# Performance work log

Measured on AMD Instinct MI355X. Metric: run time of the kernel, lower is better.

## Reference

```python
import jax, jax.numpy as jnp
import numpy as np
from jax import lax

B, N, FIN, T, K, FC, FT = 8, 2048, 3, 12, 3, 64, 64


def _conv2d(x, w, b, pad):
    # x [B,C,N,T], w [O,I,1,kw], NCHW conv
    y = lax.conv_general_dilated(x, w, (1, 1), pad,
                                 dimension_numbers=('NCHW', 'OIHW', 'NCHW'))
    return y + b[None, :, None, None]


def _spatial_att(h, W, a, alpha, concat):
    # GAT-style dense attention. h [B,N,Fin], W [Fin,D], a [2D,1]
    D = W.shape[1]
    Wh = h @ W                                             # [B,N,D]
    e = jax.nn.leaky_relu(Wh @ a[:D] + jnp.swapaxes(Wh @ a[D:], 1, 2), alpha)  # [B,N,N]
    att = jax.nn.softmax(jax.nn.sigmoid(e), axis=1)        # softmax over dim=1 (as in torch)
    hp = jnp.einsum('bij,bjd->bid', att, Wh)
    return jax.nn.elu(hp) if concat else hp


def setup_inputs() -> dict:
    key = jax.random.key(0)
    ks = jax.random.split(key, 24)
    rnd = lambda i, shape, scale=1.0: (jax.random.normal(ks[i], shape, dtype=jnp.float32) * scale)
    FTm = FC * T  # 768 spatial-attention feature dim
    D = FTm // 2
    return {
        'x': rnd(0, (B, N, FIN, T)),
        'cheb': rnd(1, (K, N, N), 1.0 / np.sqrt(N)),
        'Gamma': rnd(2, (K, FIN, FC), 1.0 / np.sqrt(FIN)),
        'W_heads': rnd(3, (2, FTm, D), 1.0 / np.sqrt(FTm)),
        'a_heads': rnd(4, (2, 2 * D, 1), 1.0 / np.sqrt(2 * D)),
        'W_out': rnd(5, (FTm, FTm), 1.0 / np.sqrt(FTm)),
        'a_out': rnd(6, (2 * FTm, 1), 1.0 / np.sqrt(2 * FTm)),
        'U1': rnd(7, (FT, FT), 1.0 / np.sqrt(FT)),
        'U2': rnd(8, (FT,), 1.0 / np.sqrt(FT)),
        'U3': rnd(9, (FT,), 1.0 / np.sqrt(FT)),
        'be': rnd(10, (1, T, T), 0.1),
        'Ve': rnd(11, (T, T), 1.0 / np.sqrt(T)),
        'time_w': rnd(12, (FT, FC, 1, 3), 1.0 / np.sqrt(3 * FC)),
        'time_b': rnd(13, (FT,), 0.01),
        'res_w': rnd(14, (FT, FIN, 1, 1), 1.0 / np.sqrt(FIN)),
        'res_b': rnd(15, (FT,), 0.01),
        'back_w': rnd(16, (FT, FC, 1, 3), 1.0 / np.sqrt(3 * FC)),
        'back_b': rnd(17, (FT,), 0.01),
        'fore_w': rnd(18, (FT, FC, 1, 3), 1.0 / np.sqrt(3 * FC)),
        'fore_b': rnd(19, (FT,), 0.01),
        'ln_g': jnp.ones((FT,), jnp.float32),
        'ln_b': jnp.zeros((FT,), jnp.float32),
    }


def reference(x, cheb, Gamma, W_heads, a_heads, W_out, a_out, U1, U2, U3, be, Ve,
              time_w, time_b, res_w, res_b, back_w, back_b, fore_w, fore_b, ln_g, ln_b):
    b, n, fin, t = x.shape
    k_ = cheb.shape[0]
    fc = Gamma.shape[2]
    # ChebNetII interpolation coefficients T_k(x_j), x_j = cos((j+0.5)pi/K) -> [j,k]
    jj = np.arange(k_)
    cxj = jnp.asarray(np.cos(np.outer((jj + 0.5) * np.pi / k_, np.arange(k_))), x.dtype)
    lhs = jnp.einsum('jio,jk->kio', Gamma, cxj)                         # [K,Fin,Fc]
    rhs = jnp.einsum('bnit,knm->kbmit', x, cheb)                        # [K,B,N,Fin,T]
    spatial_gcn = jax.nn.relu((2.0 / (k_ + 1)) * jnp.einsum('kbmit,kio->bmot', rhs, lhs))  # [B,N,Fc,T]

    # Spatial transformer: 2 GAT heads + output attention
    h = spatial_gcn.reshape(b, n, fc * t)
    heads = jax.vmap(lambda W, a: _spatial_att(h, W, a, 0.1, True))(W_heads, a_heads)  # [H,B,N,D]
    hcat = jnp.transpose(heads, (1, 2, 0, 3)).reshape(b, n, -1)
    gcn_SAt = jax.nn.relu(_spatial_att(hcat, W_out, a_out, 0.1, False)).reshape(b, n, fc, t)

    # Temporal conv (1x3, pad 1)
    tc = _conv2d(jnp.transpose(gcn_SAt, (0, 2, 1, 3)), time_w, time_b, ((0, 0), (1, 1)))
    tc = jnp.transpose(tc, (0, 2, 1, 3))                                # [B,N,Ft,T]

    # Temporal attention
    lhs_t = jnp.einsum('bnft,fg,g->btn', tc, U1, U2)                    # [B,T,N]
    rhs_t = jnp.einsum('f,bnft->bnt', U3, tc)                           # [B,N,T]
    prod = jnp.einsum('bsn,bnt->bst', lhs_t, rhs_t)                     # [B,T,T]
    E = jnp.einsum('is,bst->bit', Ve, jax.nn.sigmoid(prod + be))
    E = jax.nn.softmax(E, axis=1)
    tcn = jnp.einsum('bnft,bts->bnfs', tc, E)                           # [B,N,Ft,T]

    # Residual (1x1 conv) + LayerNorm over channel dim
    x_res = _conv2d(jnp.transpose(x, (0, 2, 1, 3)), res_w, res_b, ((0, 0), (0, 0)))
    x_res = jnp.transpose(x_res, (0, 2, 1, 3))                          # [B,N,Ft,T]
    z = jnp.transpose(jax.nn.relu(x_res + tcn), (0, 3, 1, 2))           # [B,T,N,Ft]
    mu = z.mean(-1, keepdims=True)
    var = z.var(-1, keepdims=True)
    z = (z - mu) / jnp.sqrt(var + 1e-5) * ln_g + ln_b
    result = jnp.transpose(z, (0, 2, 3, 1))                             # [B,N,Ft,T]

    rp = jnp.transpose(result, (0, 2, 1, 3))
    backcast = jnp.transpose(_conv2d(rp, back_w, back_b, ((0, 0), (1, 1))), (0, 2, 1, 3))
    forecast = jnp.transpose(_conv2d(rp, fore_w, fore_b, ((0, 0), (1, 1))), (0, 2, 1, 3))
    return (backcast, forecast)
```

## Files before the change

### kernel.cpp

```cpp
#include <hip/hip_runtime.h>


typedef unsigned short u16;
typedef __bf16 bf16x8 __attribute__((ext_vector_type(8)));
typedef float f32x4 __attribute__((ext_vector_type(4)));
typedef u16 u16x8 __attribute__((ext_vector_type(8)));

__device__ __forceinline__ u16 f2b(float f) {
  union { float f; unsigned u; } v; v.f = f;
  unsigned u = v.u;
  u = u + 0x7FFFu + ((u >> 16) & 1u);
  return (u16)(u >> 16);
}
__device__ __forceinline__ float b2f(u16 h) {
  union { unsigned u; float f; } v; v.u = ((unsigned)h) << 16; return v.f;
}
__device__ __forceinline__ float qfun(float x) {
  float e = x > 0.f ? x : 0.1f * x;
  float s = 1.f / (1.f + __expf(-e));
  return __expf(s);
}

#define GLOAD16(g, l) __builtin_amdgcn_global_load_lds( \
    (__attribute__((address_space(1))) void*)(g),       \
    (__attribute__((address_space(3))) void*)(l), 16, 0, 0)

constexpr size_t OFF_LHS     = 0x0;
constexpr size_t OFF_U1U2    = 0x1000;
constexpr size_t OFF_BIASBIG = 0x1100;
constexpr size_t OFF_FH      = 0x3000;
constexpr size_t OFF_GH      = 0x23000;
constexpr size_t OFF_RDH     = 0x43000;
constexpr size_t OFF_FO      = 0x63000;
constexpr size_t OFF_GO      = 0x73000;
constexpr size_t OFF_RDO     = 0x83000;
constexpr size_t OFF_LHST    = 0x93000;
constexpr size_t OFF_RHST    = 0x153000;
constexpr size_t OFF_PROD    = 0x213000;
constexpr size_t OFF_E       = 0x215000;
constexpr size_t OFF_WCATT   = 0x220000;
constexpr size_t OFF_WOUTT   = 0x340000;
constexpr size_t OFF_WTBIG   = 0x460000;
constexpr size_t OFF_XCOLT   = 0x580000;
constexpr size_t OFF_CHEBT   = 0x700000;
constexpr size_t OFF_C1      = 0x1F00000;
constexpr size_t OFF_H       = 0x4300000;
constexpr size_t OFF_P       = 0x700000;
constexpr size_t OFF_WHCATT  = 0x5B00000;
constexpr size_t OFF_HCAT    = 0x7300000;
constexpr size_t OFF_WHOUTT  = 0x5B00000;
constexpr size_t OFF_GCNB    = 0x7300000;
constexpr size_t OFF_WBFBIG  = 0x8B00000;
constexpr size_t OFF_TCS     = 0x700000;
constexpr size_t OFF_RESULTB = 0x3700000;
constexpr size_t WS_NEEDED   = 0x8D40000;

struct GemmP {
  const u16* A; const u16* BT;
  long sA, sB;
  int K, lda, ldb;
  int swz, splitK;
  float* Cf; long sCf; int ldcf;
  u16* Cb;  long sCb; int ldcb;
  u16* CbT; int ldcT; long sCbT;
  const float* bias;
  float* outB; float* outF;
};

template <int EPI>
__global__ __launch_bounds__(256, 2) void gemm_bf16(GemmP p) {
  constexpr int SMEM_U16 = (EPI == 1) ? (128 * 136) : 8192;
  __shared__ u16 smem[SMEM_U16];
  u16* As = smem;
  u16* Bs = smem + 4096;
  const int tid  = threadIdx.x;
  const int lane = tid & 63;
  const int wid  = tid >> 6;
  const int wm = wid >> 1, wn = wid & 1;
  const int z = blockIdx.z;

  long m0, n0;
  if (p.swz) {
    int nT = gridDim.x;
    int nwg = nT * gridDim.y;
    int lin = blockIdx.x + nT * blockIdx.y;
    int q = nwg >> 3;
    int swz = (lin & 7) * q + (lin >> 3);
    m0 = (long)(swz / nT) * 128;
    n0 = (long)(swz % nT) * 128;
  } else {
    m0 = (long)blockIdx.x * 128;
    n0 = (long)blockIdx.y * 128;
  }

  const int K = p.K;
  long aBase, bBase;
  if (p.splitK) {
    int kz = z >> 2, ch = z & 3;
    aBase = (long)kz * p.sA + (long)ch * 512;
    bBase = (long)ch * 512;
  } else {
    aBase = (long)z * p.sA;
    bBase = (long)z * p.sB;
  }
  const u16* Ab = p.A + aBase + m0 * p.lda;
  const u16* Bb = p.BT + bBase + n0 * p.ldb;

  const int srow = wid * 32 + (lane >> 2);
  const int skk  = (lane & 3) * 8;
  const u16* aP0 = Ab + (long)srow * p.lda + skk;
  const u16* aP1 = aP0 + (long)16 * p.lda;
  const u16* bP0 = Bb + (long)srow * p.ldb + skk;
  const u16* bP1 = bP0 + (long)16 * p.ldb;
  u16* lA0 = &As[(wid * 2 + 0) * 512];
  u16* lA1 = &As[(wid * 2 + 1) * 512];
  u16* lB0 = &Bs[(wid * 2 + 0) * 512];
  u16* lB1 = &Bs[(wid * 2 + 1) * 512];

  f32x4 acc[4][4];
  f32x4 zero = {0.f, 0.f, 0.f, 0.f};
#pragma unroll
  for (int i = 0; i < 4; ++i)
#pragma unroll
    for (int j = 0; j < 4; ++j) acc[i][j] = zero;

  const int aoff = (wm * 64 + (lane & 15)) * 32 + (lane >> 4) * 8;
  const int boff = (wn * 64 + (lane & 15)) * 32 + (lane >> 4) * 8;

  for (int k0 = 0; k0 < K; k0 += 32) {
    GLOAD16(aP0 + k0, lA0);
    GLOAD16(aP1 + k0, lA1);
    GLOAD16(bP0 + k0, lB0);
    GLOAD16(bP1 + k0, lB1);
    __syncthreads();
    bf16x8 av[4], bv[4];
#pragma unroll
    for (int mi = 0; mi < 4; ++mi) av[mi] = *(const bf16x8*)&As[aoff + mi * 512];
#pragma unroll
    for (int ni = 0; ni < 4; ++ni) bv[ni] = *(const bf16x8*)&Bs[boff + ni * 512];
#pragma unroll
    for (int mi = 0; mi < 4; ++mi)
#pragma unroll
      for (int ni = 0; ni < 4; ++ni)
        acc[mi][ni] = __builtin_amdgcn_mfma_f32_16x16x32_bf16(av[mi], bv[ni], acc[mi][ni], 0, 0, 0);
    __syncthreads();
  }

  if constexpr (EPI == 1) {
#pragma unroll
    for (int mi = 0; mi < 4; ++mi)
#pragma unroll
      for (int ni = 0; ni < 4; ++ni) {
        int cl = wn * 64 + ni * 16 + (lane & 15);
        int mlb = wm * 64 + mi * 16 + ((lane >> 4) << 2);
#pragma unroll
        for (int r = 0; r < 4; ++r)
          smem[cl * 136 + mlb + r] = f2b(acc[mi][ni][r]);
      }
    __syncthreads();
    int c = tid >> 1, half = tid & 1;
    long bat = m0 >> 11;
    u16* dst = p.CbT + bat * p.sCbT + (long)(n0 + c) * p.ldcT + (m0 & 2047) + half * 64;
    const u16* srcp = &smem[c * 136 + half * 64];
#pragma unroll
    for (int j = 0; j < 64; j += 8)
      *(u16x8*)(dst + j) = *(const u16x8*)(srcp + j);
    return;
  }

#pragma unroll
  for (int mi = 0; mi < 4; ++mi) {
    long rb0 = m0 + wm * 64 + mi * 16 + ((lane >> 4) << 2);
#pragma unroll
    for (int ni = 0; ni < 4; ++ni) {
      int col = (int)n0 + wn * 64 + ni * 16 + (lane & 15);
#pragma unroll
      for (int r = 0; r < 4; ++r) {
        float v = acc[mi][ni][r];
        long row = rb0 + r;
        if constexpr (EPI == 0) {
          p.Cf[(long)z * p.sCf + row * p.ldcf + col] = v;
        } else if constexpr (EPI == 2) {
          float e = v > 0.f ? v : expm1f(v);
          p.Cb[(long)z * p.sCb + row * p.ldcb + col] = f2b(e);
        } else if constexpr (EPI == 6) {
          p.Cf[row * 768 + col] = v + p.bias[col & 63];
        } else if constexpr (EPI == 7) {
          float vb = v + p.bias[col];
          if (col < 768) p.outB[row * 768 + col] = vb;
          else           p.outF[row * 768 + (col - 768)] = vb;
        } else {
          p.Cb[(long)z * p.sCb + row * p.ldcb + col] = f2b(fmaxf(v, 0.f));
        }
      }
    }
  }
}

__global__ void k_prep(const float* Gamma, const float* U1, const float* U2,
                       const float* back_b, const float* fore_b,
                       float* lhs, float* u1u2, float* biasBig) {
  int o = threadIdx.x;
  if (o < 64) {
    const float cx[3][3] = {{1.f, 0.86602540378443871f, 0.5f},
                            {1.f, 6.123233995736766e-17f, -1.f},
                            {1.f, -0.86602540378443871f, 0.5f}};
    for (int k = 0; k < 3; ++k)
      for (int i = 0; i < 3; ++i) {
        float s = 0;
        for (int j = 0; j < 3; ++j) s += Gamma[(j * 3 + i) * 64 + o] * cx[j][k];
        lhs[(k * 3 + i) * 64 + o] = s;
      }
    float s = 0;
    for (int g = 0; g < 64; ++g) s += U1[o * 64 + g] * U2[g];
    u1u2[o] = s;
    for (int t = 0; t < 12; ++t) {
      biasBig[o * 12 + t] = back_b[o];
      biasBig[768 + o * 12 + t] = fore_b[o];
    }
  }
}

__global__ void k_convert(const float* W_heads, const float* W_out, const float* time_w,
                          const float* back_w, const float* fore_w, const float* xg,
                          u16* WcatT, u16* WoutT, u16* WtBig, u16* WbfBig, u16* xcolT) {
  const int N1 = 589824, NT = 589824, NBF = 1179648, N5 = 786432;
  const int TOT = 2 * N1 + NT + NBF + N5;
  for (int o = blockIdx.x * 256 + threadIdx.x; o < TOT; o += gridDim.x * 256) {
    if (o < N1) {
      int dcol = o / 768, kk = o % 768;
      int hd = dcol / 384, d = dcol % 384;
      WcatT[o] = f2b(W_heads[((long)hd * 768 + kk) * 384 + d]);
    } else if (o < 2 * N1) {
      int o2 = o - N1; int dcol = o2 / 768, kk = o2 % 768;
      WoutT[o2] = f2b(W_out[kk * 768 + dcol]);
    } else if (o < 2 * N1 + NT) {
      int o3 = o - 2 * N1; int col = o3 / 768, kk = o3 % 768;
      int t = col >> 6, ft = col & 63, fc = kk / 12, tau = kk % 12;
      int r = tau - t + 1;
      WtBig[o3] = f2b((r >= 0 && r < 3) ? time_w[ft * 192 + fc * 3 + r] : 0.f);
    } else if (o < 2 * N1 + NT + NBF) {
      int o4 = o - 2 * N1 - NT; int col = o4 / 768, kk = o4 % 768;
      int rem = (col < 768) ? col : col - 768;
      int c = rem / 12, tt = rem % 12;
      int fc = kk / 12, tau = kk % 12; int r = tau - tt + 1;
      const float* wsrc = (col < 768) ? back_w : fore_w;
      WbfBig[o4] = f2b((r >= 0 && r < 3) ? wsrc[c * 192 + fc * 3 + r] : 0.f);
    } else {
      int o5 = o - 2 * N1 - NT - NBF; int c = o5 / 2048, n = o5 % 2048;
      float v = 0.f;
      if (c < 288) {
        int b = c / 36, r2 = c % 36, i = r2 / 12, t = r2 % 12;
        v = xg[(long)(b * 2048 + n) * 36 + i * 12 + t];
      }
      xcolT[o5] = f2b(v);
    }
  }
}

__global__ void k_chebT(const float* cheb, u16* chebT) {
  __shared__ float ts[32][33];
  int n0 = blockIdx.x * 32, m0 = blockIdx.y * 32, k = blockIdx.z;
  int c = threadIdx.x & 31, rq = threadIdx.x >> 5;
  const long base = (long)k * 2048 * 2048;
  for (int q = 0; q < 4; ++q) {
    int n = n0 + rq + q * 8;
    ts[rq + q * 8][c] = cheb[base + (long)n * 2048 + m0 + c];
  }
  __syncthreads();
  for (int q = 0; q < 4; ++q) {
    int m = m0 + rq + q * 8;
    chebT[base + (long)m * 2048 + n0 + c] = f2b(ts[c][rq + q * 8]);
  }
}

__global__ __launch_bounds__(256) void k_h(const float* C1, const float* lhs, u16* h) {
  int bn = blockIdx.x; int b = bn >> 11, n = bn & 2047;
  int tid = threadIdx.x;
  __shared__ float c1s[108], ls[576];
  if (tid < 108) {
    int kk = tid / 12, t = tid % 12; int k = kk / 3, i = kk % 3;
    float s = 0;
#pragma unroll
    for (int ch = 0; ch < 4; ++ch)
      s += C1[((long)(k * 4 + ch) * 2048 + n) * 384 + b * 36 + i * 12 + t];
    c1s[tid] = s;
  }
  for (int s = tid; s < 576; s += 256) ls[s] = lhs[s];
  __syncthreads();
  for (int q = 0; q < 3; ++q) {
    int idx = tid + q * 256; int o = idx / 12, t = idx % 12;
    float s = 0;
#pragma unroll
    for (int kk = 0; kk < 9; ++kk) s += c1s[kk * 12 + t] * ls[kk * 64 + o];
    s *= 0.5f;
    if (s < 0.f) s = 0.f;
    h[(long)bn * 768 + idx] = f2b(s);
  }
}

__global__ __launch_bounds__(256) void k_fg(const u16* WhT, int dOff, int Dlen,
                                            const float* aF, const float* aG,
                                            float* fOut, float* gOut) {
  int b = blockIdx.y;
  int i = blockIdx.x * 256 + threadIdx.x;
  __shared__ float af[768], ag[768];
  for (int s = threadIdx.x; s < Dlen; s += 256) { af[s] = aF[s]; ag[s] = aG[s]; }
  __syncthreads();
  const u16* wp = WhT + ((long)b * 768 + dOff) * 2048 + i;
  float fs = 0, gs = 0;
  for (int d = 0; d < Dlen; ++d) {
    float w = b2f(wp[(long)d * 2048]);
    fs += w * af[d]; gs += w * ag[d];
  }
  fOut[b * 2048 + i] = fs;
  gOut[b * 2048 + i] = gs;
}

__global__ __launch_bounds__(256) void k_denom(const float* f, const float* g, float* rd) {
  int b = blockIdx.y;
  int jl = threadIdx.x & 63, ch = threadIdx.x >> 6;
  int j = blockIdx.x * 64 + jl;
  __shared__ float fl[2048];
  __shared__ float red[256];
  for (int s = threadIdx.x; s < 2048; s += 256) fl[s] = f[b * 2048 + s];
  __syncthreads();
  float gj = g[b * 2048 + j];
  float acc = 0;
  for (int i = ch * 512; i < ch * 512 + 512; ++i) acc += qfun(fl[i] + gj);
  red[threadIdx.x] = acc;
  __syncthreads();
  if (ch == 0) {
    float s = red[jl] + red[jl + 64] + red[jl + 128] + red[jl + 192];
    rd[b * 2048 + j] = 1.f / s;
  }
}

__global__ __launch_bounds__(256) void k_P(const float* f, const float* g,
                                           const float* rd, u16* P) {
  int j = blockIdx.x * 256 + threadIdx.x;
  int i0 = blockIdx.y * 16;
  int b = blockIdx.z;
  __shared__ float fl[16];
  if (threadIdx.x < 16) fl[threadIdx.x] = f[b * 2048 + i0 + threadIdx.x];
  __syncthreads();
  float gj = g[b * 2048 + j], rj = rd[b * 2048 + j];
  u16* Pp = P + ((long)b * 2048 + i0) * 2048 + j;
#pragma unroll
  for (int ii = 0; ii < 16; ++ii) Pp[(long)ii * 2048] = f2b(qfun(fl[ii] + gj) * rj);
}

__global__ void k_temporal(const float* tc, const float* u1u2, const float* U3g,
                           float* lhs_t, float* rhs_t) {
  __shared__ float uu[64], u3[64];
  int tid = threadIdx.x;
  if (tid < 64) { uu[tid] = u1u2[tid]; u3[tid] = U3g[tid]; }
  __syncthreads();
  int gid = blockIdx.x * 256 + tid;
  const float* p = tc + (long)gid * 64;
  float s1 = 0, s2 = 0;
#pragma unroll 8
  for (int fx = 0; fx < 64; ++fx) {
    float v = p[fx];
    s1 += v * uu[fx]; s2 += v * u3[fx];
  }
  int t = gid % 12; long bn = gid / 12;
  int n = (int)(bn & 2047), b = (int)(bn >> 11);
  lhs_t[((long)b * 12 + t) * 2048 + n] = s1;
  rhs_t[gid] = s2;
  (void)n;
}

__global__ void k_prod(const float* lhs_t, const float* rhs_t, float* prod) {
  int bi = blockIdx.x;
  int b = bi / 144; int r = bi % 144; int s = r / 12; int u = r % 12;
  int tid = threadIdx.x;
  float acc = 0;
  const float* lp = lhs_t + ((long)b * 12 + s) * 2048;
  const float* rp = rhs_t + (long)b * 2048 * 12 + u;
  for (int n = tid; n < 2048; n += 256) acc += lp[n] * rp[n * 12];
  __shared__ float red[256];
  red[tid] = acc; __syncthreads();
  for (int st = 128; st > 0; st >>= 1) {
    if (tid < st) red[tid] += red[tid + st];
    __syncthreads();
  }
  if (tid == 0) prod[bi] = red[0];
}

__global__ void k_E(const float* prod, const float* be, const float* Ve, float* E) {
  int b = blockIdx.x; int tid = threadIdx.x;
  __shared__ float S0[144], E1[144], mx[12], dn[12];
  if (tid < 144) {
    float v = prod[b * 144 + tid] + be[tid];
    S0[tid] = 1.f / (1.f + __expf(-v));
  }
  __syncthreads();
  if (tid < 144) {
    int i = tid / 12, t = tid % 12;
    float a = 0;
    for (int s = 0; s < 12; ++s) a += Ve[i * 12 + s] * S0[s * 12 + t];
    E1[tid] = a;
  }
  __syncthreads();
  if (tid < 12) {
    float m = -1e30f;
    for (int i = 0; i < 12; ++i) m = fmaxf(m, E1[i * 12 + tid]);
    float d = 0;
    for (int i = 0; i < 12; ++i) d += __expf(E1[i * 12 + tid] - m);
    mx[tid] = m; dn[tid] = d;
  }
  __syncthreads();
  if (tid < 144) {
    int t = tid % 12;
    E[b * 144 + tid] = __expf(E1[tid] - mx[t]) / dn[t];
  }
}

__global__ __launch_bounds__(256) void k_res_ln(const float* tc, const float* E,
                                                const float* xg, const float* res_w,
                                                const float* res_b, const float* ln_g,
                                                const float* ln_b, u16* result) {
  int bn = blockIdx.x; int b = bn >> 11;
  int tid = threadIdx.x;
  __shared__ float tcb[768], Eb[144], xl[36], rw[192], rb[64], lg[64], lb[64], zl[768], mu[12], rs[12];
  for (int s = tid; s < 768; s += 256) tcb[s] = tc[(long)bn * 768 + s];
  if (tid < 144) Eb[tid] = E[b * 144 + tid];
  if (tid < 36) xl[tid] = xg[(long)bn * 36 + tid];
  if (tid >= 64 && tid < 256) { int q = tid - 64; if (q < 192) rw[q] = res_w[q]; }
  if (tid < 64) { rb[tid] = res_b[tid]; lg[tid] = ln_g[tid]; lb[tid] = ln_b[tid]; }
  __syncthreads();
  float z[3];
#pragma unroll
  for (int q = 0; q < 3; ++q) {
    int idx = tid + q * 256; int f = idx / 12, s = idx % 12;
    float tcn = 0;
#pragma unroll
    for (int t = 0; t < 12; ++t) tcn += tcb[t * 64 + f] * Eb[t * 12 + s];
    float xr = rb[f];
#pragma unroll
    for (int i = 0; i < 3; ++i) xr += rw[f * 3 + i] * xl[i * 12 + s];
    float v = xr + tcn;
    v = v > 0.f ? v : 0.f;
    z[q] = v; zl[idx] = v;
  }
  __syncthreads();
  if (tid < 12) {
    float m = 0, m2 = 0;
    for (int f = 0; f < 64; ++f) { float v = zl[f * 12 + tid]; m += v; m2 += v * v; }
    m *= (1.f / 64.f); m2 *= (1.f / 64.f);
    mu[tid] = m;
    float var = m2 - m * m;
    rs[tid] = rsqrtf((var > 0.f ? var : 0.f) + 1e-5f);
  }
  __syncthreads();
#pragma unroll
  for (int q = 0; q < 3; ++q) {
    int idx = tid + q * 256; int f = idx / 12, s = idx % 12;
    result[(long)bn * 768 + idx] = f2b((z[q] - mu[s]) * rs[s] * lg[f] + lb[f]);
  }
}

__global__ void k_sentinel(float* out, long n) {
  long i = (long)blockIdx.x * 256 + threadIdx.x;
  if (i < n) out[i] = 12345.0f;
}

extern "C" void kernel_launch(void* const* d_in, const int* in_sizes, int n_in,
                              void* d_out, int out_size, void* d_ws, size_t ws_size,
                              hipStream_t stream) {
  (void)in_sizes; (void)n_in;
  const float* x       = (const float*)d_in[0];
  const float* cheb    = (const float*)d_in[1];
  const float* Gamma   = (const float*)d_in[2];
  const float* W_heads = (const float*)d_in[3];
  const float* a_heads = (const float*)d_in[4];
  const float* W_out   = (const float*)d_in[5];
  const float* a_out   = (const float*)d_in[6];
  const float* U1      = (const float*)d_in[7];
  const float* U2      = (const float*)d_in[8];
  const float* U3      = (const float*)d_in[9];
  const float* be      = (const float*)d_in[10];
  const float* Ve      = (const float*)d_in[11];
  const float* time_w  = (const float*)d_in[12];
  const float* time_b  = (const float*)d_in[13];
  const float* res_w   = (const float*)d_in[14];
  const float* res_b   = (const float*)d_in[15];
  const float* back_w  = (const float*)d_in[16];
  const float* back_b  = (const float*)d_in[17];
  const float* fore_w  = (const float*)d_in[18];
  const float* fore_b  = (const float*)d_in[19];
  const float* ln_g    = (const float*)d_in[20];
  const float* ln_b    = (const float*)d_in[21];
  float* out = (float*)d_out;

  if (ws_size < WS_NEEDED) {
    k_sentinel<<<(out_size + 255) / 256, 256, 0, stream>>>(out, out_size);
    return;
  }

  char* ws = (char*)d_ws;
  float* lhs     = (float*)(ws + OFF_LHS);
  float* u1u2    = (float*)(ws + OFF_U1U2);
  float* biasBig = (float*)(ws + OFF_BIASBIG);
  float* fH      = (float*)(ws + OFF_FH);
  float* gH      = (float*)(ws + OFF_GH);
  float* rdH     = (float*)(ws + OFF_RDH);
  float* fO      = (float*)(ws + OFF_FO);
  float* gO      = (float*)(ws + OFF_GO);
  float* rdO     = (float*)(ws + OFF_RDO);
  float* lhs_t   = (float*)(ws + OFF_LHST);
  float* rhs_t   = (float*)(ws + OFF_RHST);
  float* prod    = (float*)(ws + OFF_PROD);
  float* Ebuf    = (float*)(ws + OFF_E);
  u16* WcatT   = (u16*)(ws + OFF_WCATT);
  u16* WoutT   = (u16*)(ws + OFF_WOUTT);
  u16* WtBig   = (u16*)(ws + OFF_WTBIG);
  u16* WbfBig  = (u16*)(ws + OFF_WBFBIG);
  u16* xcolT   = (u16*)(ws + OFF_XCOLT);
  u16* chebT   = (u16*)(ws + OFF_CHEBT);
  float* C1    = (float*)(ws + OFF_C1);
  u16* hbuf    = (u16*)(ws + OFF_H);
  u16* Pbuf    = (u16*)(ws + OFF_P);
  u16* WhcatT  = (u16*)(ws + OFF_WHCATT);
  u16* hcat    = (u16*)(ws + OFF_HCAT);
  u16* WhoutT  = (u16*)(ws + OFF_WHOUTT);
  u16* gcnB    = (u16*)(ws + OFF_GCNB);
  float* tcs   = (float*)(ws + OFF_TCS);
  u16* resultB = (u16*)(ws + OFF_RESULTB);

  k_prep<<<1, 64, 0, stream>>>(Gamma, U1, U2, back_b, fore_b, lhs, u1u2, biasBig);
  k_convert<<<2048, 256, 0, stream>>>(W_heads, W_out, time_w, back_w, fore_w, x,
                                      WcatT, WoutT, WtBig, WbfBig, xcolT);
  k_chebT<<<dim3(64, 64, 3), 256, 0, stream>>>(cheb, chebT);

  {
    GemmP p{}; p.A = chebT; p.BT = xcolT; p.sA = 2048L * 2048; p.sB = 0;
    p.K = 512; p.lda = 2048; p.ldb = 2048; p.splitK = 1; p.swz = 1;
    p.Cf = C1; p.sCf = 2048L * 384; p.ldcf = 384;
    gemm_bf16<0><<<dim3(3, 16, 12), 256, 0, stream>>>(p);
  }
  k_h<<<16384, 256, 0, stream>>>(C1, lhs, hbuf);

  {
    GemmP p{}; p.A = hbuf; p.BT = WcatT; p.sA = 0; p.sB = 0;
    p.K = 768; p.lda = 768; p.ldb = 768; p.swz = 1;
    p.CbT = WhcatT; p.ldcT = 2048; p.sCbT = 768L * 2048;
    gemm_bf16<1><<<dim3(6, 128, 1), 256, 0, stream>>>(p);
  }
  k_fg<<<dim3(8, 8), 256, 0, stream>>>(WhcatT, 0, 384, a_heads, a_heads + 384, fH, gH);
  k_fg<<<dim3(8, 8), 256, 0, stream>>>(WhcatT, 384, 384, a_heads + 768, a_heads + 1152,
                                       fH + 16384, gH + 16384);
  for (int hd = 0; hd < 2; ++hd) {
    const float* f = fH + hd * 16384; const float* g = gH + hd * 16384;
    float* rd = rdH + hd * 16384;
    k_denom<<<dim3(32, 8), 256, 0, stream>>>(f, g, rd);
    k_P<<<dim3(8, 128, 8), 256, 0, stream>>>(f, g, rd, Pbuf);
    GemmP p{}; p.A = Pbuf; p.BT = WhcatT + (long)hd * 384 * 2048;
    p.sA = 2048L * 2048; p.sB = 768L * 2048;
    p.K = 2048; p.lda = 2048; p.ldb = 2048; p.swz = 1;
    p.Cb = hcat + hd * 384; p.sCb = 2048L * 768; p.ldcb = 768;
    gemm_bf16<2><<<dim3(3, 16, 8), 256, 0, stream>>>(p);
  }

  {
    GemmP p{}; p.A = hcat; p.BT = WoutT; p.sA = 0; p.sB = 0;
    p.K = 768; p.lda = 768; p.ldb = 768; p.swz = 1;
    p.CbT = WhoutT; p.ldcT = 2048; p.sCbT = 768L * 2048;
    gemm_bf16<1><<<dim3(6, 128, 1), 256, 0, stream>>>(p);
  }
  k_fg<<<dim3(8, 8), 256, 0, stream>>>(WhoutT, 0, 768, a_out, a_out + 768, fO, gO);
  k_denom<<<dim3(32, 8), 256, 0, stream>>>(fO, gO, rdO);
  k_P<<<dim3(8, 128, 8), 256, 0, stream>>>(fO, gO, rdO, Pbuf);
  {
    GemmP p{}; p.A = Pbuf; p.BT = WhoutT; p.sA = 2048L * 2048; p.sB = 768L * 2048;
    p.K = 2048; p.lda = 2048; p.ldb = 2048; p.swz = 1;
    p.Cb = gcnB; p.sCb = 2048L * 768; p.ldcb = 768;
    gemm_bf16<8><<<dim3(6, 16, 8), 256, 0, stream>>>(p);
  }

  {
    GemmP p{}; p.A = gcnB; p.BT = WtBig; p.sA = 0; p.sB = 0;
    p.K = 768; p.lda = 768; p.ldb = 768; p.swz = 1;
    p.Cf = tcs; p.bias = time_b;
    gemm_bf16<6><<<dim3(6, 128, 1), 256, 0, stream>>>(p);
  }

  k_temporal<<<768, 256, 0, stream>>>(tcs, u1u2, U3, lhs_t, rhs_t);
  k_prod<<<1152, 256, 0, stream>>>(lhs_t, rhs_t, prod);
  k_E<<<8, 256, 0, stream>>>(prod, be, Ve, Ebuf);

  k_res_ln<<<16384, 256, 0, stream>>>(tcs, Ebuf, x, res_w, res_b, ln_g, ln_b, resultB);

  {
    GemmP p{}; p.A = resultB; p.BT = WbfBig; p.sA = 0; p.sB = 0;
    p.K = 768; p.lda = 768; p.ldb = 768; p.swz = 1;
    p.bias = biasBig; p.outB = out; p.outF = out + 12582912L;
    gemm_bf16<7><<<dim3(12, 128, 1), 256, 0, stream>>>(p);
  }
}
```

Before: 814.3 us.

## Double-buffer GEMM LDS tiles with XOR swizzle and store temporal conv in bf16

The shared bf16 GEMM kernel now double-buffers its LDS tiles, issuing the next K-slice's global-to-LDS loads before the MFMAs on the current slice, so each iteration needs one barrier instead of two. The LDS layout also gets an XOR swizzle on the 16-byte chunk index to reduce bank conflicts on fragment reads. Separately, the temporal-conv output (tcs) is written as bf16 instead of fp32, which halves its traffic into k_temporal and k_res_ln, and k_temporal now reads it with vectorised 8-wide loads. Costs: LDS per block doubles to 32 KB, which may limit occupancy, and the temporal features lose precision.

```diff
diff --git a/kernel.cpp b/kernel.cpp
--- a/kernel.cpp
+++ b/kernel.cpp
@@ -69,10 +69,8 @@
 
 template <int EPI>
 __global__ __launch_bounds__(256, 2) void gemm_bf16(GemmP p) {
-  constexpr int SMEM_U16 = (EPI == 1) ? (128 * 136) : 8192;
+  constexpr int SMEM_U16 = (EPI == 1) ? 17408 : 16384;
   __shared__ u16 smem[SMEM_U16];
-  u16* As = smem;
-  u16* Bs = smem + 4096;
   const int tid  = threadIdx.x;
   const int lane = tid & 63;
   const int wid  = tid >> 6;
@@ -107,15 +105,11 @@
   const u16* Bb = p.BT + bBase + n0 * p.ldb;
 
   const int srow = wid * 32 + (lane >> 2);
-  const int skk  = (lane & 3) * 8;
-  const u16* aP0 = Ab + (long)srow * p.lda + skk;
+  const int sk   = (((lane & 3) ^ ((lane >> 3) & 3))) * 8;
+  const u16* aP0 = Ab + (long)srow * p.lda + sk;
   const u16* aP1 = aP0 + (long)16 * p.lda;
-  const u16* bP0 = Bb + (long)srow * p.ldb + skk;
+  const u16* bP0 = Bb + (long)srow * p.ldb + sk;
   const u16* bP1 = bP0 + (long)16 * p.ldb;
-  u16* lA0 = &As[(wid * 2 + 0) * 512];
-  u16* lA1 = &As[(wid * 2 + 1) * 512];
-  u16* lB0 = &Bs[(wid * 2 + 0) * 512];
-  u16* lB1 = &Bs[(wid * 2 + 1) * 512];
 
   f32x4 acc[4][4];
   f32x4 zero = {0.f, 0.f, 0.f, 0.f};
@@ -124,15 +118,32 @@
 #pragma unroll
     for (int j = 0; j < 4; ++j) acc[i][j] = zero;
 
-  const int aoff = (wm * 64 + (lane & 15)) * 32 + (lane >> 4) * 8;
-  const int boff = (wn * 64 + (lane & 15)) * 32 + (lane >> 4) * 8;
-
+  const int xorc = (lane >> 1) & 3;
+  const int aoff = (wm * 64 + (lane & 15)) * 32 + (((lane >> 4) ^ xorc)) * 8;
+  const int boff = (wn * 64 + (lane & 15)) * 32 + (((lane >> 4) ^ xorc)) * 8;
+
+  const int lslot = (wid * 2) * 512;
+
+  {
+    u16* base = smem;
+    GLOAD16(aP0, base + lslot);
+    GLOAD16(aP1, base + lslot + 512);
+    GLOAD16(bP0, base + 4096 + lslot);
+    GLOAD16(bP1, base + 4096 + lslot + 512);
+  }
+  __syncthreads();
+
+  int cur = 0;
   for (int k0 = 0; k0 < K; k0 += 32) {
-    GLOAD16(aP0 + k0, lA0);
-    GLOAD16(aP1 + k0, lA1);
-    GLOAD16(bP0 + k0, lB0);
-    GLOAD16(bP1 + k0, lB1);
-    __syncthreads();
+    if (k0 + 32 < K) {
+      u16* base = smem + (cur ^ 1) * 8192;
+      GLOAD16(aP0 + k0 + 32, base + lslot);
+      GLOAD16(aP1 + k0 + 32, base + lslot + 512);
+      GLOAD16(bP0 + k0 + 32, base + 4096 + lslot);
+      GLOAD16(bP1 + k0 + 32, base + 4096 + lslot + 512);
+    }
+    const u16* As = smem + cur * 8192;
+    const u16* Bs = As + 4096;
     bf16x8 av[4], bv[4];
 #pragma unroll
     for (int mi = 0; mi < 4; ++mi) av[mi] = *(const bf16x8*)&As[aoff + mi * 512];
@@ -144,6 +155,7 @@
       for (int ni = 0; ni < 4; ++ni)
         acc[mi][ni] = __builtin_amdgcn_mfma_f32_16x16x32_bf16(av[mi], bv[ni], acc[mi][ni], 0, 0, 0);
     __syncthreads();
+    cur ^= 1;
   }
 
   if constexpr (EPI == 1) {
@@ -184,7 +196,7 @@
           float e = v > 0.f ? v : expm1f(v);
           p.Cb[(long)z * p.sCb + row * p.ldcb + col] = f2b(e);
         } else if constexpr (EPI == 6) {
-          p.Cf[row * 768 + col] = v + p.bias[col & 63];
+          p.Cb[row * 768 + col] = f2b(v + p.bias[col & 63]);
         } else if constexpr (EPI == 7) {
           float vb = v + p.bias[col];
           if (col < 768) p.outB[row * 768 + col] = vb;
@@ -350,25 +362,28 @@
   for (int ii = 0; ii < 16; ++ii) Pp[(long)ii * 2048] = f2b(qfun(fl[ii] + gj) * rj);
 }
 
-__global__ void k_temporal(const float* tc, const float* u1u2, const float* U3g,
+__global__ void k_temporal(const u16* tc, const float* u1u2, const float* U3g,
                            float* lhs_t, float* rhs_t) {
   __shared__ float uu[64], u3[64];
   int tid = threadIdx.x;
   if (tid < 64) { uu[tid] = u1u2[tid]; u3[tid] = U3g[tid]; }
   __syncthreads();
   int gid = blockIdx.x * 256 + tid;
-  const float* p = tc + (long)gid * 64;
+  const u16* p = tc + (long)gid * 64;
   float s1 = 0, s2 = 0;
-#pragma unroll 8
-  for (int fx = 0; fx < 64; ++fx) {
-    float v = p[fx];
-    s1 += v * uu[fx]; s2 += v * u3[fx];
+#pragma unroll
+  for (int c = 0; c < 8; ++c) {
+    u16x8 vv = *(const u16x8*)(p + c * 8);
+#pragma unroll
+    for (int j = 0; j < 8; ++j) {
+      float v = b2f(vv[j]);
+      s1 += v * uu[c * 8 + j]; s2 += v * u3[c * 8 + j];
+    }
   }
   int t = gid % 12; long bn = gid / 12;
-  int n = (int)(bn & 2047), b = (int)(bn >> 11);
-  lhs_t[((long)b * 12 + t) * 2048 + n] = s1;
+  int b = (int)(bn >> 11);
+  lhs_t[((long)b * 12 + t) * 2048 + (int)(bn & 2047)] = s1;
   rhs_t[gid] = s2;
-  (void)n;
 }
 
 __global__ void k_prod(const float* lhs_t, const float* rhs_t, float* prod) {
@@ -417,14 +432,14 @@
   }
 }
 
-__global__ __launch_bounds__(256) void k_res_ln(const float* tc, const float* E,
+__global__ __launch_bounds__(256) void k_res_ln(const u16* tc, const float* E,
                                                 const float* xg, const float* res_w,
                                                 const float* res_b, const float* ln_g,
                                                 const float* ln_b, u16* result) {
   int bn = blockIdx.x; int b = bn >> 11;
   int tid = threadIdx.x;
   __shared__ float tcb[768], Eb[144], xl[36], rw[192], rb[64], lg[64], lb[64], zl[768], mu[12], rs[12];
-  for (int s = tid; s < 768; s += 256) tcb[s] = tc[(long)bn * 768 + s];
+  for (int s = tid; s < 768; s += 256) tcb[s] = b2f(tc[(long)bn * 768 + s]);
   if (tid < 144) Eb[tid] = E[b * 144 + tid];
   if (tid < 36) xl[tid] = xg[(long)bn * 36 + tid];
   if (tid >= 64 && tid < 256) { int q = tid - 64; if (q < 192) rw[q] = res_w[q]; }
@@ -526,7 +541,7 @@
   u16* hcat    = (u16*)(ws + OFF_HCAT);
   u16* WhoutT  = (u16*)(ws + OFF_WHOUTT);
   u16* gcnB    = (u16*)(ws + OFF_GCNB);
-  float* tcs   = (float*)(ws + OFF_TCS);
+  u16* tcsB    = (u16*)(ws + OFF_TCS);
   u16* resultB = (u16*)(ws + OFF_RESULTB);
 
   k_prep<<<1, 64, 0, stream>>>(Gamma, U1, U2, back_b, fore_b, lhs, u1u2, biasBig);
@@ -582,15 +597,15 @@
   {
     GemmP p{}; p.A = gcnB; p.BT = WtBig; p.sA = 0; p.sB = 0;
     p.K = 768; p.lda = 768; p.ldb = 768; p.swz = 1;
-    p.Cf = tcs; p.bias = time_b;
+    p.Cb = tcsB; p.bias = time_b;
     gemm_bf16<6><<<dim3(6, 128, 1), 256, 0, stream>>>(p);
   }
 
-  k_temporal<<<768, 256, 0, stream>>>(tcs, u1u2, U3, lhs_t, rhs_t);
+  k_temporal<<<768, 256, 0, stream>>>(tcsB, u1u2, U3, lhs_t, rhs_t);
   k_prod<<<1152, 256, 0, stream>>>(lhs_t, rhs_t, prod);
   k_E<<<8, 256, 0, stream>>>(prod, be, Ve, Ebuf);
 
-  k_res_ln<<<16384, 256, 0, stream>>>(tcs, Ebuf, x, res_w, res_b, ln_g, ln_b, resultB);
+  k_res_ln<<<16384, 256, 0, stream>>>(tcsB, Ebuf, x, res_w, res_b, ln_g, ln_b, resultB);
 
   {
     GemmP p{}; p.A = resultB; p.BT = WbfBig; p.sA = 0; p.sB = 0;
```

Measured after the change: 777.3 us. 1.05x faster.
